# Optimization experiments

Measured on AMD Instinct MI355X. Metric: run time of the kernel, lower is better.

The kernel has to match this reference:

```python
import jax, jax.numpy as jnp
import numpy as np


def _fo_pool(f, z):
    # c_t = f_t * c_{t-1} + z_t, c_0 = 0, scanned over axis 1 (seq).
    # Associative combine: (a1,b1) * (a2,b2) = (a1*a2, a2*b1 + b2)
    def combine(left, right):
        a1, b1 = left
        a2, b2 = right
        return a1 * a2, a2 * b1 + b2
    _, c = jax.lax.associative_scan(combine, (f, z), axis=1)
    return c


def setup_inputs() -> dict:
    key = jax.random.key(0)
    ks = jax.random.split(key, 10)
    B, S, D_in, D_model, D_mlp, n_cls = 32, 2048, 512, 1024, 1024, 128
    s = 0.02
    return {
        "x":  jax.random.normal(ks[0], (B, S, D_in), dtype=jnp.float32),
        "W":  jax.random.normal(ks[1], (D_in, 3 * D_model), dtype=jnp.float32) * s,  # Linear, bias=False
        "V":  jax.random.normal(ks[2], (D_in, 3 * D_model), dtype=jnp.float32) * s,
        "Vb": jax.random.normal(ks[3], (3 * D_model,), dtype=jnp.float32) * s,
        "W0": jax.random.normal(ks[4], (D_model, D_mlp), dtype=jnp.float32) * s,
        "b0": jax.random.normal(ks[5], (D_mlp,), dtype=jnp.float32) * s,
        "W1": jax.random.normal(ks[6], (D_mlp, D_mlp), dtype=jnp.float32) * s,
        "b1": jax.random.normal(ks[7], (D_mlp,), dtype=jnp.float32) * s,
        "W2": jax.random.normal(ks[8], (D_mlp, n_cls), dtype=jnp.float32) * s,
        "b2": jax.random.normal(ks[9], (n_cls,), dtype=jnp.float32) * s,
    }


def reference(x, W, V, Vb, W0, b0, W1, b1, W2, b2):
    # kernel_size=2 pre: W(x) + V(x shifted right by one, zero-padded)
    xprev = jnp.pad(x[:, :-1, :], ((0, 0), (1, 0), (0, 0)))  # [B,S,D_in]
    pre = jnp.einsum('bsd,dk->bsk', x, W) + jnp.einsum('bsd,dk->bsk', xprev, V) + Vb
    f, z, o = jnp.split(pre, 3, axis=-1)
    f = jax.nn.sigmoid(f)
    z = (1.0 - f) * jnp.tanh(z)
    o = jax.nn.sigmoid(o)
    c = _fo_pool(f, z)          # [B,S,D_model]
    h = c * o
    q = h[:, -1, :]             # last timestep
    # dropout is identity at inference (training=False)
    q = jax.nn.relu(q @ W0 + b0)
    q = jax.nn.relu(q @ W1 + b1)
    return q @ W2 + b2
```

## Files before the change

### kernel.cpp

```cpp
#include <hip/hip_runtime.h>
#include <cstdint>
#include <cstddef>


typedef __attribute__((ext_vector_type(8))) short short8;
typedef __attribute__((ext_vector_type(4))) float f32x4;

__device__ __forceinline__ unsigned short f2bf(float f) {
  unsigned int u = __float_as_uint(f);
  u += 0x7fffu + ((u >> 16) & 1u);
  return (unsigned short)(u >> 16);
}

__device__ __forceinline__ void gload_lds16(const void* g, void* l) {
  __builtin_amdgcn_global_load_lds(
      (const __attribute__((address_space(1))) unsigned int*)g,
      (__attribute__((address_space(3))) unsigned int*)l, 16, 0, 0);
}

__device__ __forceinline__ float sigmoidf_fast(float x) {
  return 1.f / (1.f + __expf(-x));
}
__device__ __forceinline__ float tanhf_fast(float x) {
  float a = fabsf(x);
  float e = __expf(-2.f * a);
  float t = (1.f - e) / (1.f + e);
  return copysignf(t, x);
}

__global__ void pack_x_kernel(const float* __restrict__ x, unsigned short* __restrict__ xb) {
  int gid = blockIdx.x * 256 + threadIdx.x;
  float4 v = ((const float4*)x)[gid];
  ushort4 o;
  o.x = f2bf(v.x); o.y = f2bf(v.y); o.z = f2bf(v.z); o.w = f2bf(v.w);
  ((ushort4*)xb)[gid] = o;
}

__global__ void pack_u_kernel(const float* __restrict__ W, const float* __restrict__ V,
                              unsigned short* __restrict__ U) {
  __shared__ float T[64 * 65];
  const int j0 = blockIdx.x * 64;
  const int k0 = blockIdx.y * 64;
  const int jl = threadIdx.x & 63;
  const int q  = threadIdx.x >> 6;
  const float* src = (k0 < 512) ? (W + (size_t)k0 * 3072) : (V + (size_t)(k0 - 512) * 3072);
#pragma unroll 4
  for (int i = 0; i < 16; ++i) {
    int kl = q * 16 + i;
    T[kl * 65 + jl] = src[(size_t)kl * 3072 + j0 + jl];
  }
  __syncthreads();
  const int kl = threadIdx.x & 63;
#pragma unroll 4
  for (int i = 0; i < 16; ++i) {
    int jj = q * 16 + i;
    U[(size_t)(j0 + jj) * 1024 + k0 + kl] = f2bf(T[kl * 65 + jj]);
  }
}

__global__ __launch_bounds__(256) void qrnn_main(
    const unsigned short* __restrict__ xb, const float* __restrict__ xf, int use_bf,
    const unsigned short* __restrict__ U, const float* __restrict__ Vb,
    float* __restrict__ Fagg, float* __restrict__ Zagg) {
  __shared__ __align__(16) char smem[50176];
  char* As = smem;
  char* Us = smem + 17408;

  const int dt = blockIdx.x;
  const int cj = blockIdx.y;
  const int b  = blockIdx.z;
  const int tid = threadIdx.x;
  const int lane = tid & 63;
  const int wid  = tid >> 6;
  const int wm = wid >> 1, wn = wid & 1;
  const int s0 = cj * 128;

  f32x4 acc[4][4];
#pragma unroll
  for (int i = 0; i < 4; ++i)
#pragma unroll
    for (int j = 0; j < 4; ++j) acc[i][j] = f32x4{0.f, 0.f, 0.f, 0.f};

  const int mrow = wm * 64 + (lane & 15);
  const int ncol = wn * 64 + (lane & 15);
  const int rloc = lane >> 3;
  const int pc   = lane & 7;
  const int frow = tid >> 3;
  const int fc   = tid & 7;

  for (int kt = 0; kt < 8; ++kt) {
    __syncthreads();
    if (use_bf) {
#pragma unroll
      for (int p = 0; p < 4; ++p) {
        int rr = wid * 32 + p * 8 + rloc;
        int c = pc ^ (rr & 7);
        ptrdiff_t s = (ptrdiff_t)b * 2048 + (s0 - 1 + rr);
        gload_lds16(xb + s * 512 + kt * 64 + c * 8, As + (wid * 32 + p * 8) * 128);
      }
      if (tid < 8) {
        gload_lds16(xb + ((size_t)b * 2048 + s0 + 127) * 512 + kt * 64 + tid * 8,
                    As + 128 * 128);
      }
    } else {
#pragma unroll
      for (int p = 0; p < 4; ++p) {
        int rr = frow + p * 32;
        int s = s0 - 1 + rr;
        uint4 v = make_uint4(0u, 0u, 0u, 0u);
        if (s >= 0) {
          const float* src = xf + (((size_t)b * 2048 + s) << 9) + kt * 64 + fc * 8;
          float4 a0 = *(const float4*)src;
          float4 a1 = *(const float4*)(src + 4);
          v.x = (unsigned)f2bf(a0.x) | ((unsigned)f2bf(a0.y) << 16);
          v.y = (unsigned)f2bf(a0.z) | ((unsigned)f2bf(a0.w) << 16);
          v.z = (unsigned)f2bf(a1.x) | ((unsigned)f2bf(a1.y) << 16);
          v.w = (unsigned)f2bf(a1.z) | ((unsigned)f2bf(a1.w) << 16);
        }
        *(uint4*)(As + rr * 128 + ((fc ^ (rr & 7)) << 4)) = v;
      }
      if (tid < 8) {
        const float* src = xf + (((size_t)b * 2048 + s0 + 127) << 9) + kt * 64 + tid * 8;
        float4 a0 = *(const float4*)src;
        float4 a1 = *(const float4*)(src + 4);
        uint4 v;
        v.x = (unsigned)f2bf(a0.x) | ((unsigned)f2bf(a0.y) << 16);
        v.y = (unsigned)f2bf(a0.z) | ((unsigned)f2bf(a0.w) << 16);
        v.z = (unsigned)f2bf(a1.x) | ((unsigned)f2bf(a1.y) << 16);
        v.w = (unsigned)f2bf(a1.z) | ((unsigned)f2bf(a1.w) << 16);
        *(uint4*)(As + 128 * 128 + (tid << 4)) = v;
      }
    }
#pragma unroll
    for (int h2 = 0; h2 < 2; ++h2)
#pragma unroll
      for (int p = 0; p < 4; ++p) {
        int cc = wid * 32 + p * 8 + rloc;
        int j = (cc < 64) ? (dt * 64 + cc) : (1024 + dt * 64 + (cc - 64));
        int c = pc ^ (cc & 7);
        gload_lds16(U + ((size_t)j << 10) + h2 * 512 + kt * 64 + c * 8,
                    Us + h2 * 16384 + (wid * 32 + p * 8) * 128);
      }
    __syncthreads();
    if (cj == 0) {
      if (tid < 8) *(uint4*)(As + (tid << 4)) = make_uint4(0u, 0u, 0u, 0u);
      __syncthreads();
    }
#pragma unroll
    for (int h2 = 0; h2 < 2; ++h2) {
      const char* Ub = Us + h2 * 16384;
#pragma unroll
      for (int kb = 0; kb < 2; ++kb) {
        const int cbase = kb * 4 + (lane >> 4);
        short8 afr[4], bfr[4];
#pragma unroll
        for (int i = 0; i < 4; ++i) {
          int rr = mrow + i * 16 + 1 - h2;
          afr[i] = *(const short8*)(As + rr * 128 + ((cbase ^ (rr & 7)) << 4));
          int n = ncol + i * 16;
          bfr[i] = *(const short8*)(Ub + n * 128 + ((cbase ^ (n & 7)) << 4));
        }
#pragma unroll
        for (int mt = 0; mt < 4; ++mt)
#pragma unroll
          for (int nt = 0; nt < 4; ++nt)
            acc[mt][nt] = __builtin_amdgcn_mfma_f32_16x16x32_bf16(afr[mt], bfr[nt], acc[mt][nt], 0, 0, 0);
      }
    }
  }

  float* fA   = (float*)smem;
  float* tzA  = (float*)(smem + 17408);
  float* segF = (float*)(smem + 34816);
  float* segZ = (float*)(smem + 35840);

  const int d = tid & 63;
  const int dl = lane & 15;
  float vb[4];
#pragma unroll
  for (int nt = 0; nt < 4; ++nt)
    vb[nt] = Vb[wn * 1024 + dt * 64 + nt * 16 + dl];

  float F_run = 1.f, Z_run = 0.f;

  for (int ph = 0; ph < 2; ++ph) {
    __syncthreads();
    if (wm == ph) {
      float* dst = (wn == 0) ? fA : tzA;
#pragma unroll
      for (int mt = 0; mt < 4; ++mt)
#pragma unroll
        for (int nt = 0; nt < 4; ++nt)
#pragma unroll
          for (int rg = 0; rg < 4; ++rg) {
            int t = mt * 16 + ((lane >> 4) << 2) + rg;
            int c = nt * 16 + dl;
            float v = acc[mt][nt][rg] + vb[nt];
            v = (wn == 0) ? sigmoidf_fast(v) : tanhf_fast(v);
            dst[t * 68 + c] = v;
          }
    }
    __syncthreads();
    {
      int seg = tid >> 6;
      float F = 1.f, Z = 0.f;
#pragma unroll 4
      for (int i = 0; i < 16; ++i) {
        int t = seg * 16 + i;
        float f  = fA[t * 68 + d];
        float tz = tzA[t * 68 + d];
        float z = (1.f - f) * tz;
        Z = f * Z + z;
        F *= f;
      }
      segF[seg * 64 + d] = F;
      segZ[seg * 64 + d] = Z;
    }
    __syncthreads();
    if (tid < 64) {
#pragma unroll
      for (int sgi = 0; sgi < 4; ++sgi) {
        float Fs = segF[sgi * 64 + tid], Zs = segZ[sgi * 64 + tid];
        Z_run = Fs * Z_run + Zs;
        F_run *= Fs;
      }
    }
  }
  if (tid < 64) {
    size_t o = ((size_t)b * 16 + cj) * 1024 + dt * 64 + tid;
    Fagg[o] = F_run;
    Zagg[o] = Z_run;
  }
}

__global__ void head_kernel(const float* __restrict__ x, const float* __restrict__ W,
                            const float* __restrict__ V, const float* __restrict__ Vb,
                            const float* __restrict__ Fagg, const float* __restrict__ Zagg,
                            float* __restrict__ h) {
  __shared__ float red[4][64];
  const int dl = threadIdx.x & 63;
  const int w  = threadIdx.x >> 6;
  const int d = blockIdx.x * 64 + dl;
  const int b = blockIdx.y;

  const float* xl = x + ((size_t)b * 2048 + 2047) * 512;
  const float* xp = xl - 512;
  const float* Wc = W + 2048 + d;
  const float* Vc = V + 2048 + d;
  float po = 0.f;
  const int k0 = w * 128;
#pragma unroll 8
  for (int k = k0; k < k0 + 128; ++k) {
    po += xl[k] * Wc[(size_t)k * 3072];
    po += xp[k] * Vc[(size_t)k * 3072];
  }
  red[w][dl] = po;
  __syncthreads();
  if (w == 0) {
    po = red[0][dl] + red[1][dl] + red[2][dl] + red[3][dl] + Vb[2048 + d];
    float c = 0.f;
#pragma unroll
    for (int j = 0; j < 16; ++j) {
      size_t o = (((size_t)b * 16 + j) << 10) + d;
      c = Fagg[o] * c + Zagg[o];
    }
    h[((size_t)b << 10) + d] = c * sigmoidf_fast(po);
  }
}

__global__ void mlp_kernel(const float* __restrict__ in, const float* __restrict__ Wt,
                           const float* __restrict__ bias, float* __restrict__ out,
                           int K, int N, int do_relu) {
  __shared__ float red[4][64];
  const int nl = threadIdx.x & 63;
  const int w  = threadIdx.x >> 6;
  const int n = blockIdx.x * 64 + nl;
  const int b = blockIdx.y;
  const float* row = in + (size_t)b * K;
  const float* Wc = Wt + n;
  float s = 0.f;
  const int kq = K >> 2;
  const int k0 = w * kq;
#pragma unroll 8
  for (int k = k0; k < k0 + kq; ++k) s += row[k] * Wc[(size_t)k * N];
  red[w][nl] = s;
  __syncthreads();
  if (w == 0) {
    s = red[0][nl] + red[1][nl] + red[2][nl] + red[3][nl] + bias[n];
    if (do_relu) s = fmaxf(s, 0.f);
    out[(size_t)b * N + n] = s;
  }
}

extern "C" void kernel_launch(void* const* d_in, const int* in_sizes, int n_in,
                              void* d_out, int out_size, void* d_ws, size_t ws_size,
                              hipStream_t stream) {
  const float* x  = (const float*)d_in[0];
  const float* W  = (const float*)d_in[1];
  const float* V  = (const float*)d_in[2];
  const float* Vb = (const float*)d_in[3];
  const float* W0 = (const float*)d_in[4];
  const float* b0 = (const float*)d_in[5];
  const float* W1 = (const float*)d_in[6];
  const float* b1 = (const float*)d_in[7];
  const float* W2 = (const float*)d_in[8];
  const float* b2 = (const float*)d_in[9];

  char* ws = (char*)d_ws;
  unsigned short* U = (unsigned short*)(ws);
  float* Fagg = (float*)(ws + (size_t)4 * 1024 * 1024);
  float* Zagg = (float*)(ws + (size_t)6 * 1024 * 1024);
  float* h    = (float*)(ws + (size_t)8 * 1024 * 1024);
  float* q0   = (float*)(ws + (size_t)8 * 1024 * 1024 + 256 * 1024);
  float* q1   = (float*)(ws + (size_t)8 * 1024 * 1024 + 512 * 1024);
  unsigned short* xb = (unsigned short*)(ws + (size_t)16 * 1024 * 1024);

  const size_t need_bf = (size_t)16 * 1024 * 1024 + (size_t)67108864;
  int use_bf = (ws_size >= need_bf) ? 1 : 0;

  if (use_bf) pack_x_kernel<<<32768, 256, 0, stream>>>(x, xb);
  pack_u_kernel<<<dim3(32, 16), 256, 0, stream>>>(W, V, U);
  qrnn_main<<<dim3(16, 16, 32), 256, 0, stream>>>(xb, x, use_bf, U, Vb, Fagg, Zagg);
  head_kernel<<<dim3(16, 32), 256, 0, stream>>>(x, W, V, Vb, Fagg, Zagg, h);
  mlp_kernel<<<dim3(16, 32), 256, 0, stream>>>(h, W0, b0, q0, 1024, 1024, 1);
  mlp_kernel<<<dim3(16, 32), 256, 0, stream>>>(q0, W1, b1, q1, 1024, 1024, 1);
  mlp_kernel<<<dim3(2, 32), 256, 0, stream>>>(q1, W2, b2, (float*)d_out, 1024, 128, 0);
}
```

Before: 648.9 us.

## Double QRNN sequence chunk per block and split MLP over K with atomics

The main QRNN block now runs 512 threads and covers 256 timesteps instead of 128. That halves the number of sequence chunks and reuses each U tile across twice as many rows, at the cost of more LDS per block and a longer in-block scan over four phases. The MLP layers are split four ways along K with atomicAdd into buffers pre-filled with the biases. ReLU moves to the consumer's input so each layer launches more blocks. The atomic accumulation makes summation order nondeterministic and adds an init kernel.

```diff
diff --git a/kernel.cpp b/kernel.cpp
--- a/kernel.cpp
+++ b/kernel.cpp
@@ -58,13 +58,13 @@
   }
 }
 
-__global__ __launch_bounds__(256) void qrnn_main(
+__global__ __launch_bounds__(512, 4) void qrnn_main(
     const unsigned short* __restrict__ xb, const float* __restrict__ xf, int use_bf,
     const unsigned short* __restrict__ U, const float* __restrict__ Vb,
     float* __restrict__ Fagg, float* __restrict__ Zagg) {
-  __shared__ __align__(16) char smem[50176];
+  __shared__ __align__(16) char smem[65664];
   char* As = smem;
-  char* Us = smem + 17408;
+  char* Us = smem + 32896;
 
   const int dt = blockIdx.x;
   const int cj = blockIdx.y;
@@ -73,7 +73,7 @@
   const int lane = tid & 63;
   const int wid  = tid >> 6;
   const int wm = wid >> 1, wn = wid & 1;
-  const int s0 = cj * 128;
+  const int s0 = cj * 256;
 
   f32x4 acc[4][4];
 #pragma unroll
@@ -85,8 +85,6 @@
   const int ncol = wn * 64 + (lane & 15);
   const int rloc = lane >> 3;
   const int pc   = lane & 7;
-  const int frow = tid >> 3;
-  const int fc   = tid & 7;
 
   for (int kt = 0; kt < 8; ++kt) {
     __syncthreads();
@@ -99,13 +97,23 @@
         gload_lds16(xb + s * 512 + kt * 64 + c * 8, As + (wid * 32 + p * 8) * 128);
       }
       if (tid < 8) {
-        gload_lds16(xb + ((size_t)b * 2048 + s0 + 127) * 512 + kt * 64 + tid * 8,
-                    As + 128 * 128);
+        gload_lds16(xb + ((size_t)b * 2048 + s0 + 255) * 512 + kt * 64 + tid * 8,
+                    As + 256 * 128);
+      }
+#pragma unroll
+      for (int p = 0; p < 4; ++p) {
+        int cc = wid * 32 + p * 8 + rloc;
+        int half = cc >> 7, col = cc & 127;
+        int j = (col < 64) ? (dt * 64 + col) : (1024 + dt * 64 + (col - 64));
+        int c = pc ^ (cc & 7);
+        gload_lds16(U + ((size_t)j << 10) + half * 512 + kt * 64 + c * 8,
+                    Us + (wid * 32 + p * 8) * 128);
       }
     } else {
 #pragma unroll
       for (int p = 0; p < 4; ++p) {
-        int rr = frow + p * 32;
+        int rr = (tid >> 3) + p * 64;
+        int fc = tid & 7;
         int s = s0 - 1 + rr;
         uint4 v = make_uint4(0u, 0u, 0u, 0u);
         if (s >= 0) {
@@ -120,7 +128,7 @@
         *(uint4*)(As + rr * 128 + ((fc ^ (rr & 7)) << 4)) = v;
       }
       if (tid < 8) {
-        const float* src = xf + (((size_t)b * 2048 + s0 + 127) << 9) + kt * 64 + tid * 8;
+        const float* src = xf + (((size_t)b * 2048 + s0 + 255) << 9) + kt * 64 + tid * 8;
         float4 a0 = *(const float4*)src;
         float4 a1 = *(const float4*)(src + 4);
         uint4 v;
@@ -128,19 +136,21 @@
         v.y = (unsigned)f2bf(a0.z) | ((unsigned)f2bf(a0.w) << 16);
         v.z = (unsigned)f2bf(a1.x) | ((unsigned)f2bf(a1.y) << 16);
         v.w = (unsigned)f2bf(a1.z) | ((unsigned)f2bf(a1.w) << 16);
-        *(uint4*)(As + 128 * 128 + (tid << 4)) = v;
-      }
-    }
-#pragma unroll
-    for (int h2 = 0; h2 < 2; ++h2)
-#pragma unroll
-      for (int p = 0; p < 4; ++p) {
-        int cc = wid * 32 + p * 8 + rloc;
-        int j = (cc < 64) ? (dt * 64 + cc) : (1024 + dt * 64 + (cc - 64));
-        int c = pc ^ (cc & 7);
-        gload_lds16(U + ((size_t)j << 10) + h2 * 512 + kt * 64 + c * 8,
-                    Us + h2 * 16384 + (wid * 32 + p * 8) * 128);
-      }
+        *(uint4*)(As + 256 * 128 + (tid << 4)) = v;
+      }
+      {
+#pragma unroll
+        for (int p = 0; p < 4; ++p) {
+          int cc = (tid >> 3) + p * 64;
+          int half = cc >> 7, col = cc & 127;
+          int j = (col < 64) ? (dt * 64 + col) : (1024 + dt * 64 + (col - 64));
+          int fc = tid & 7;
+          int c = fc ^ (cc & 7);
+          uint4 v = *(const uint4*)(U + ((size_t)j << 10) + half * 512 + kt * 64 + c * 8);
+          *(uint4*)(Us + cc * 128 + (fc << 4)) = v;
+        }
+      }
+    }
     __syncthreads();
     if (cj == 0) {
       if (tid < 8) *(uint4*)(As + (tid << 4)) = make_uint4(0u, 0u, 0u, 0u);
@@ -172,7 +182,7 @@
   float* fA   = (float*)smem;
   float* tzA  = (float*)(smem + 17408);
   float* segF = (float*)(smem + 34816);
-  float* segZ = (float*)(smem + 35840);
+  float* segZ = (float*)(smem + 36864);
 
   const int d = tid & 63;
   const int dl = lane & 15;
@@ -183,7 +193,7 @@
 
   float F_run = 1.f, Z_run = 0.f;
 
-  for (int ph = 0; ph < 2; ++ph) {
+  for (int ph = 0; ph < 4; ++ph) {
     __syncthreads();
     if (wm == ph) {
       float* dst = (wn == 0) ? fA : tzA;
@@ -204,9 +214,9 @@
     {
       int seg = tid >> 6;
       float F = 1.f, Z = 0.f;
-#pragma unroll 4
-      for (int i = 0; i < 16; ++i) {
-        int t = seg * 16 + i;
+#pragma unroll
+      for (int i = 0; i < 8; ++i) {
+        int t = seg * 8 + i;
         float f  = fA[t * 68 + d];
         float tz = tzA[t * 68 + d];
         float z = (1.f - f) * tz;
@@ -219,7 +229,7 @@
     __syncthreads();
     if (tid < 64) {
 #pragma unroll
-      for (int sgi = 0; sgi < 4; ++sgi) {
+      for (int sgi = 0; sgi < 8; ++sgi) {
         float Fs = segF[sgi * 64 + tid], Zs = segZ[sgi * 64 + tid];
         Z_run = Fs * Z_run + Zs;
         F_run *= Fs;
@@ -227,7 +237,7 @@
     }
   }
   if (tid < 64) {
-    size_t o = ((size_t)b * 16 + cj) * 1024 + dt * 64 + tid;
+    size_t o = (((size_t)b * 8 + cj) << 10) + dt * 64 + tid;
     Fagg[o] = F_run;
     Zagg[o] = Z_run;
   }
@@ -260,35 +270,46 @@
     po = red[0][dl] + red[1][dl] + red[2][dl] + red[3][dl] + Vb[2048 + d];
     float c = 0.f;
 #pragma unroll
-    for (int j = 0; j < 16; ++j) {
-      size_t o = (((size_t)b * 16 + j) << 10) + d;
+    for (int j = 0; j < 8; ++j) {
+      size_t o = (((size_t)b * 8 + j) << 10) + d;
       c = Fagg[o] * c + Zagg[o];
     }
     h[((size_t)b << 10) + d] = c * sigmoidf_fast(po);
   }
 }
 
-__global__ void mlp_kernel(const float* __restrict__ in, const float* __restrict__ Wt,
-                           const float* __restrict__ bias, float* __restrict__ out,
-                           int K, int N, int do_relu) {
+__global__ void init_mlp_kernel(const float* __restrict__ b0, const float* __restrict__ b1,
+                                const float* __restrict__ b2,
+                                float* __restrict__ q0, float* __restrict__ q1,
+                                float* __restrict__ out) {
+  int gid = blockIdx.x * 256 + threadIdx.x;
+  q0[gid] = b0[gid & 1023];
+  q1[gid] = b1[gid & 1023];
+  if (gid < 4096) out[gid] = b2[gid & 127];
+}
+
+__global__ void mlp_atomic_kernel(const float* __restrict__ in, const float* __restrict__ Wt,
+                                  float* __restrict__ out, int K, int N, int relu_in) {
   __shared__ float red[4][64];
   const int nl = threadIdx.x & 63;
   const int w  = threadIdx.x >> 6;
   const int n = blockIdx.x * 64 + nl;
   const int b = blockIdx.y;
+  const int k0 = blockIdx.z * (K >> 2) + w * (K >> 4);
   const float* row = in + (size_t)b * K;
   const float* Wc = Wt + n;
   float s = 0.f;
-  const int kq = K >> 2;
-  const int k0 = w * kq;
 #pragma unroll 8
-  for (int k = k0; k < k0 + kq; ++k) s += row[k] * Wc[(size_t)k * N];
+  for (int k = k0; k < k0 + (K >> 4); ++k) {
+    float v = row[k];
+    if (relu_in) v = fmaxf(v, 0.f);
+    s += v * Wc[(size_t)k * N];
+  }
   red[w][nl] = s;
   __syncthreads();
   if (w == 0) {
-    s = red[0][nl] + red[1][nl] + red[2][nl] + red[3][nl] + bias[n];
-    if (do_relu) s = fmaxf(s, 0.f);
-    out[(size_t)b * N + n] = s;
+    s = red[0][nl] + red[1][nl] + red[2][nl] + red[3][nl];
+    atomicAdd(&out[(size_t)b * N + n], s);
   }
 }
 
@@ -320,9 +341,10 @@
 
   if (use_bf) pack_x_kernel<<<32768, 256, 0, stream>>>(x, xb);
   pack_u_kernel<<<dim3(32, 16), 256, 0, stream>>>(W, V, U);
-  qrnn_main<<<dim3(16, 16, 32), 256, 0, stream>>>(xb, x, use_bf, U, Vb, Fagg, Zagg);
+  init_mlp_kernel<<<128, 256, 0, stream>>>(b0, b1, b2, q0, q1, (float*)d_out);
+  qrnn_main<<<dim3(16, 8, 32), 512, 0, stream>>>(xb, x, use_bf, U, Vb, Fagg, Zagg);
   head_kernel<<<dim3(16, 32), 256, 0, stream>>>(x, W, V, Vb, Fagg, Zagg, h);
-  mlp_kernel<<<dim3(16, 32), 256, 0, stream>>>(h, W0, b0, q0, 1024, 1024, 1);
-  mlp_kernel<<<dim3(16, 32), 256, 0, stream>>>(q0, W1, b1, q1, 1024, 1024, 1);
-  mlp_kernel<<<dim3(2, 32), 256, 0, stream>>>(q1, W2, b2, (float*)d_out, 1024, 128, 0);
-}
+  mlp_atomic_kernel<<<dim3(16, 32, 4), 256, 0, stream>>>(h, W0, q0, 1024, 1024, 0);
+  mlp_atomic_kernel<<<dim3(16, 32, 4), 256, 0, stream>>>(q0, W1, q1, 1024, 1024, 1);
+  mlp_atomic_kernel<<<dim3(2, 32, 4), 256, 0, stream>>>(q1, W2, (float*)d_out, 1024, 128, 1);
+}
```

New measurement: 637.4 us. No clear change (-1.8%).
